# Kernel optimization log

Hardware: AMD Instinct MI355X
Metric: run time of the kernel (lower is better)

## Reference

```python
import jax, jax.numpy as jnp
import numpy as np

ALPHA = 1.702
LIMIT = 7.0
H = 2880      # hidden_size
D = 2880      # expert_dim (intermediate_size)
E = 8         # num_local_experts
B, S = 1, 1024


def setup_inputs() -> dict:
    key = jax.random.key(0)
    k1, k2, k3, k4, k5, k6 = jax.random.split(key, 6)
    scale = 1.0 / np.sqrt(H)
    return {
        "hidden_states": jax.random.normal(k1, (B, S, H), dtype=jnp.float32),
        "routing_weights": jax.random.uniform(k2, (B * S, E), dtype=jnp.float32),
        "gate_up_proj": jax.random.normal(k3, (E, H, 2 * D), dtype=jnp.float32) * scale,
        "gate_up_proj_bias": jax.random.normal(k4, (E, 2 * D), dtype=jnp.float32) * 0.02,
        "down_proj": jax.random.normal(k5, (E, D, H), dtype=jnp.float32) * (1.0 / np.sqrt(D)),
        "down_proj_bias": jax.random.normal(k6, (E, H), dtype=jnp.float32) * 0.02,
    }


def reference(hidden_states, routing_weights, gate_up_proj, gate_up_proj_bias,
              down_proj, down_proj_bias):
    b, s, h = hidden_states.shape
    x = hidden_states.reshape(-1, h)                       # [T, H]
    # Dense all-experts formulation (faithful to original): every expert sees every token.
    gate_up = jnp.einsum('th,ehd->etd', x, gate_up_proj) + gate_up_proj_bias[:, None, :]  # [E,T,2D]
    gate = gate_up[..., ::2]                               # interleaved split
    up = gate_up[..., 1::2]
    gate = jnp.minimum(gate, LIMIT)
    up = jnp.clip(up, -LIMIT, LIMIT)
    glu = gate * jax.nn.sigmoid(gate * ALPHA)
    out = jnp.einsum('etd,edh->eth', (up + 1.0) * glu, down_proj) + down_proj_bias[:, None, :]  # [E,T,H]
    # combine with routing weights: routing_weights [T,E] -> [E,T,1]
    out = out * routing_weights.T[:, :, None]
    y = out.sum(axis=0)                                    # [T, H]
    return y.reshape(b, s, h)
```

## Files before the change

### kernel.cpp

```cpp
#include <hip/hip_runtime.h>

namespace {

constexpr int T     = 1024;
constexpr int HDIM  = 2880;
constexpr int DDIM  = 2880;
constexpr int NE    = 8;
constexpr int TWO_D = 5760;
constexpr float ALPHA = 1.702f;
constexpr float LIMIT = 7.0f;

constexpr int LDSS = 40;

typedef __attribute__((ext_vector_type(8))) short bf16x8;
typedef __attribute__((ext_vector_type(4))) unsigned short u16x4;
typedef __attribute__((ext_vector_type(4))) float f32x4;

__device__ __forceinline__ unsigned short f2bf(float f) {
  union { float f; unsigned u; } x; x.f = f;
  unsigned u = x.u;
  u += 0x7fffu + ((u >> 16) & 1u);
  return (unsigned short)(u >> 16);
}

__device__ __forceinline__ void async16(const void* g, void* l) {
  __builtin_amdgcn_global_load_lds(
      (const __attribute__((address_space(1))) unsigned int*)g,
      (__attribute__((address_space(3))) unsigned int*)l, 16, 0, 0);
}

}


__global__ __launch_bounds__(256) void cvt_x_kernel(const float* __restrict__ X,
                                                    unsigned short* __restrict__ Xb) {
  const int i = (blockIdx.x * 256 + threadIdx.x) * 8;
  const f32x4 a = *(const f32x4*)(X + i);
  const f32x4 b = *(const f32x4*)(X + i + 4);
  bf16x8 pv;
  pv[0] = (short)f2bf(a.x); pv[1] = (short)f2bf(a.y);
  pv[2] = (short)f2bf(a.z); pv[3] = (short)f2bf(a.w);
  pv[4] = (short)f2bf(b.x); pv[5] = (short)f2bf(b.y);
  pv[6] = (short)f2bf(b.z); pv[7] = (short)f2bf(b.w);
  *(bf16x8*)(Xb + i) = pv;
}

__global__ __launch_bounds__(256) void transpose_cvt_kernel(
    const float* __restrict__ src, unsigned short* __restrict__ dst,
    int R, int C) {
  __shared__ __align__(16) unsigned short lt[64][70];
  const size_t eo = (size_t)blockIdx.z * R * C;
  const float* sp = src + eo;
  unsigned short* dp = dst + eo;
  const int c0 = blockIdx.x * 64;
  const int r0 = blockIdx.y * 64;
  const int t  = threadIdx.x;

  const int lr = t >> 4;
  const int lc = (t & 15) * 4;
#pragma unroll
  for (int it = 0; it < 4; ++it) {
    const int rr = lr + it * 16;
    const f32x4 v = *(const f32x4*)(sp + (size_t)(r0 + rr) * C + c0 + lc);
    const unsigned w0 = (unsigned)f2bf(v.x) | ((unsigned)f2bf(v.y) << 16);
    const unsigned w1 = (unsigned)f2bf(v.z) | ((unsigned)f2bf(v.w) << 16);
    *(unsigned*)(&lt[rr][lc])     = w0;
    *(unsigned*)(&lt[rr][lc + 2]) = w1;
  }
  __syncthreads();

  const int dr  = (t & 7) * 8;
  const int dcb = t >> 3;
#pragma unroll
  for (int it = 0; it < 2; ++it) {
    const int c = dcb + it * 32;
    bf16x8 ov;
#pragma unroll
    for (int j = 0; j < 8; ++j) ov[j] = (short)lt[dr + j][c];
    *(bf16x8*)(dp + (size_t)(c0 + c) * R + r0 + dr) = ov;
  }
}

__global__ __launch_bounds__(256) void gemm1_fast(
    const unsigned short* __restrict__ Xb,
    const unsigned short* __restrict__ W1T,
    const float* __restrict__ B1,
    const float* __restrict__ RW,
    unsigned short* __restrict__ A)
{
  __shared__ __align__(16) unsigned short lA[128 * 32];
  __shared__ __align__(16) unsigned short lB[128 * 32];

  const int tid = threadIdx.x;
  const int m0 = blockIdx.x * 128;
  const int n0 = blockIdx.y * 128;
  const int e  = blockIdx.z;
  const unsigned short* Wp = W1T + (size_t)e * TWO_D * HDIM;

  f32x4 acc[4][4];
#pragma unroll
  for (int i = 0; i < 4; ++i)
#pragma unroll
    for (int j = 0; j < 4; ++j) acc[i][j] = (f32x4)0.f;

  const int w    = tid >> 6;
  const int lane = tid & 63;
  const int wm   = w & 1, wn = w >> 1;
  const int r    = lane & 15, q = lane >> 4;

  const int srow = lane >> 2;
  const int skc  = (lane & 3) * 8;
  const unsigned short* ga = Xb + (size_t)(m0 + w * 32 + srow) * HDIM + skc;
  const unsigned short* gb = Wp + (size_t)(n0 + w * 32 + srow) * HDIM + skc;
  unsigned short* la0 = lA + (w * 2) * 512;
  unsigned short* lb0 = lB + (w * 2) * 512;

  for (int kt = 0; kt < HDIM / 32; ++kt) {
    const int k0 = kt * 32;
    async16(ga + k0,                        la0);
    async16(ga + (size_t)16 * HDIM + k0,    la0 + 512);
    async16(gb + k0,                        lb0);
    async16(gb + (size_t)16 * HDIM + k0,    lb0 + 512);
    __syncthreads();

    const unsigned short* pA = &lA[(wm * 64 + r) * 32 + q * 8];
    const unsigned short* pB = &lB[(wn * 64 + r) * 32 + q * 8];
    bf16x8 af[4], bfr[4];
#pragma unroll
    for (int i = 0; i < 4; ++i) af[i]  = *(const bf16x8*)(pA + i * 512);
#pragma unroll
    for (int j = 0; j < 4; ++j) bfr[j] = *(const bf16x8*)(pB + j * 512);
#pragma unroll
    for (int i = 0; i < 4; ++i)
#pragma unroll
      for (int j = 0; j < 4; ++j)
        acc[i][j] = __builtin_amdgcn_mfma_f32_16x16x32_bf16(af[i], bfr[j], acc[i][j], 0, 0, 0);

    __syncthreads();
  }

  const float* bp = B1 + (size_t)e * TWO_D;
#pragma unroll
  for (int i = 0; i < 4; ++i) {
    const int mb = m0 + wm * 64 + i * 16 + q * 4;
    float rwv[4];
#pragma unroll
    for (int p = 0; p < 4; ++p) rwv[p] = RW[(mb + p) * NE + e];
#pragma unroll
    for (int j = 0; j < 4; ++j) {
      const int c = n0 + wn * 64 + j * 16 + r;
      const float bias = bp[c];
#pragma unroll
      for (int p = 0; p < 4; ++p) {
        float v = acc[i][j][p] + bias;
        float o = __shfl_xor(v, 1, 64);
        float gate = (r & 1) ? o : v;
        float up   = (r & 1) ? v : o;
        gate = fminf(gate, LIMIT);
        up   = fminf(fmaxf(up, -LIMIT), LIMIT);
        float glu = gate / (1.f + __expf(-ALPHA * gate));
        float a   = (up + 1.f) * glu * rwv[p];
        if ((r & 1) == 0) {
          int d = c >> 1;
          A[(size_t)e * T * DDIM + (size_t)(mb + p) * DDIM + d] = f2bf(a);
        }
      }
    }
  }
}

__global__ __launch_bounds__(256) void gemm2_fast(
    const unsigned short* __restrict__ A,
    const unsigned short* __restrict__ W2T,
    float* __restrict__ Yp)
{
  __shared__ __align__(16) unsigned short lA[128 * 32];
  __shared__ __align__(16) unsigned short lB[128 * 32];

  const int tid = threadIdx.x;
  const int m0 = blockIdx.x * 128;
  const int n0 = blockIdx.y * 128;
  const int e  = blockIdx.z;
  const unsigned short* Ap = A   + (size_t)e * T * DDIM;
  const unsigned short* Wp = W2T + (size_t)e * HDIM * DDIM;

  f32x4 acc[4][4];
#pragma unroll
  for (int i = 0; i < 4; ++i)
#pragma unroll
    for (int j = 0; j < 4; ++j) acc[i][j] = (f32x4)0.f;

  const int w    = tid >> 6;
  const int lane = tid & 63;
  const int wm   = w & 1, wn = w >> 1;
  const int r    = lane & 15, q = lane >> 4;

  const int srow = lane >> 2;
  const int skc  = (lane & 3) * 8;
  int br0 = n0 + w * 32 + srow;
  int br1 = br0 + 16;
  if (br0 > HDIM - 1) br0 = HDIM - 1;
  if (br1 > HDIM - 1) br1 = HDIM - 1;
  const unsigned short* ga  = Ap + (size_t)(m0 + w * 32 + srow) * DDIM + skc;
  const unsigned short* gb0 = Wp + (size_t)br0 * DDIM + skc;
  const unsigned short* gb1 = Wp + (size_t)br1 * DDIM + skc;
  unsigned short* la0 = lA + (w * 2) * 512;
  unsigned short* lb0 = lB + (w * 2) * 512;

  for (int kt = 0; kt < DDIM / 32; ++kt) {
    const int k0 = kt * 32;
    async16(ga  + k0,                     la0);
    async16(ga  + (size_t)16 * DDIM + k0, la0 + 512);
    async16(gb0 + k0,                     lb0);
    async16(gb1 + k0,                     lb0 + 512);
    __syncthreads();

    const unsigned short* pA = &lA[(wm * 64 + r) * 32 + q * 8];
    const unsigned short* pB = &lB[(wn * 64 + r) * 32 + q * 8];
    bf16x8 af[4], bfr[4];
#pragma unroll
    for (int i = 0; i < 4; ++i) af[i]  = *(const bf16x8*)(pA + i * 512);
#pragma unroll
    for (int j = 0; j < 4; ++j) bfr[j] = *(const bf16x8*)(pB + j * 512);
#pragma unroll
    for (int i = 0; i < 4; ++i)
#pragma unroll
      for (int j = 0; j < 4; ++j)
        acc[i][j] = __builtin_amdgcn_mfma_f32_16x16x32_bf16(af[i], bfr[j], acc[i][j], 0, 0, 0);

    __syncthreads();
  }

#pragma unroll
  for (int i = 0; i < 4; ++i) {
    const int mb = m0 + wm * 64 + i * 16 + q * 4;
#pragma unroll
    for (int j = 0; j < 4; ++j) {
      const int h = n0 + wn * 64 + j * 16 + r;
      if (h < HDIM) {
#pragma unroll
        for (int p = 0; p < 4; ++p)
          Yp[((size_t)e * T + (mb + p)) * HDIM + h] = acc[i][j][p];
      }
    }
  }
}

__global__ __launch_bounds__(256) void reduce_bias_kernel(
    const float* __restrict__ Yp, const float* __restrict__ RW,
    const float* __restrict__ B2, float* __restrict__ Y) {
  const int idx = (blockIdx.x * 256 + threadIdx.x) * 4;
  const int t = idx / HDIM;
  const int h = idx - t * HDIM;
  f32x4 s = (f32x4)0.f;
#pragma unroll
  for (int e = 0; e < NE; ++e) {
    const f32x4 v = *(const f32x4*)(Yp + ((size_t)e * T + t) * HDIM + h);
    const f32x4 b = *(const f32x4*)(B2 + (size_t)e * HDIM + h);
    const float rw = RW[t * NE + e];
    s.x += v.x + rw * b.x;
    s.y += v.y + rw * b.y;
    s.z += v.z + rw * b.z;
    s.w += v.w + rw * b.w;
  }
  *(f32x4*)(Y + idx) = s;
}


__global__ void init_bias_kernel(const float* __restrict__ RW,
                                 const float* __restrict__ B2,
                                 float* __restrict__ Y) {
  int h = blockIdx.x * 64 + threadIdx.x;
  int t = blockIdx.y;
  float s = 0.f;
#pragma unroll
  for (int e = 0; e < NE; ++e) s += RW[t * NE + e] * B2[e * HDIM + h];
  Y[(size_t)t * HDIM + h] = s;
}

__global__ __launch_bounds__(256) void gemm1_act_kernel(
    const float* __restrict__ X, const float* __restrict__ W1,
    const float* __restrict__ B1, const float* __restrict__ RW,
    unsigned short* __restrict__ A) {
  __shared__ __align__(16) unsigned short lA[128 * LDSS];
  __shared__ __align__(16) unsigned short lB[128 * LDSS];
  const int tid = threadIdx.x;
  const int m0 = blockIdx.x * 128;
  const int n0 = blockIdx.y * 128;
  const int e  = blockIdx.z;
  const float* Wp = W1 + (size_t)e * HDIM * TWO_D;
  f32x4 acc[4][4];
#pragma unroll
  for (int i = 0; i < 4; ++i)
#pragma unroll
    for (int j = 0; j < 4; ++j) acc[i][j] = (f32x4)0.f;
  const int w = tid >> 6, lane = tid & 63;
  const int wm = w & 1, wn = w >> 1;
  const int r = lane & 15, q = lane >> 4;
  const int sa_m = tid >> 3, sa_q = tid & 7;
  const int sb_n = tid & 127, sb_k = tid >> 7;
  for (int kt = 0; kt < HDIM / 32; ++kt) {
    const int k0g = kt * 32;
#pragma unroll
    for (int it = 0; it < 4; ++it) {
      int m = sa_m + it * 32;
      const f32x4 v = *(const f32x4*)(X + (size_t)(m0 + m) * HDIM + k0g + sa_q * 4);
      u16x4 pv = { f2bf(v.x), f2bf(v.y), f2bf(v.z), f2bf(v.w) };
      *(u16x4*)(&lA[m * LDSS + sa_q * 4]) = pv;
    }
#pragma unroll
    for (int it = 0; it < 2; ++it) {
      int k0 = (sb_k + it * 2) * 8;
      float f[8];
#pragma unroll
      for (int rr = 0; rr < 8; ++rr)
        f[rr] = Wp[(size_t)(k0g + k0 + rr) * TWO_D + n0 + sb_n];
      bf16x8 pv = { (short)f2bf(f[0]), (short)f2bf(f[1]), (short)f2bf(f[2]), (short)f2bf(f[3]),
                    (short)f2bf(f[4]), (short)f2bf(f[5]), (short)f2bf(f[6]), (short)f2bf(f[7]) };
      *(bf16x8*)(&lB[sb_n * LDSS + k0]) = pv;
    }
    __syncthreads();
    const unsigned short* pA = &lA[(wm * 64 + r) * LDSS + q * 8];
    const unsigned short* pB = &lB[(wn * 64 + r) * LDSS + q * 8];
    bf16x8 af[4], bfr[4];
#pragma unroll
    for (int i = 0; i < 4; ++i) af[i]  = *(const bf16x8*)(pA + i * 16 * LDSS);
#pragma unroll
    for (int j = 0; j < 4; ++j) bfr[j] = *(const bf16x8*)(pB + j * 16 * LDSS);
#pragma unroll
    for (int i = 0; i < 4; ++i)
#pragma unroll
      for (int j = 0; j < 4; ++j)
        acc[i][j] = __builtin_amdgcn_mfma_f32_16x16x32_bf16(af[i], bfr[j], acc[i][j], 0, 0, 0);
    __syncthreads();
  }
  const float* bp = B1 + (size_t)e * TWO_D;
#pragma unroll
  for (int i = 0; i < 4; ++i) {
    const int mb = m0 + wm * 64 + i * 16 + q * 4;
    float rwv[4];
#pragma unroll
    for (int p = 0; p < 4; ++p) rwv[p] = RW[(mb + p) * NE + e];
#pragma unroll
    for (int j = 0; j < 4; ++j) {
      const int c = n0 + wn * 64 + j * 16 + r;
      const float bias = bp[c];
#pragma unroll
      for (int p = 0; p < 4; ++p) {
        float v = acc[i][j][p] + bias;
        float o = __shfl_xor(v, 1, 64);
        float gate = (r & 1) ? o : v;
        float up   = (r & 1) ? v : o;
        gate = fminf(gate, LIMIT);
        up   = fminf(fmaxf(up, -LIMIT), LIMIT);
        float glu = gate / (1.f + __expf(-ALPHA * gate));
        float a   = (up + 1.f) * glu * rwv[p];
        if ((r & 1) == 0) {
          int d = c >> 1;
          A[(size_t)e * T * DDIM + (size_t)(mb + p) * DDIM + d] = f2bf(a);
        }
      }
    }
  }
}

__global__ __launch_bounds__(256) void gemm2_acc_kernel(
    const unsigned short* __restrict__ A, const float* __restrict__ W2,
    float* __restrict__ Y) {
  __shared__ __align__(16) unsigned short lA[128 * LDSS];
  __shared__ __align__(16) unsigned short lB[128 * LDSS];
  const int tid = threadIdx.x;
  const int m0 = blockIdx.x * 128;
  const int n0 = blockIdx.y * 128;
  const int e  = blockIdx.z;
  const float* Wp = W2 + (size_t)e * DDIM * HDIM;
  const unsigned short* Ap = A + (size_t)e * T * DDIM;
  f32x4 acc[4][4];
#pragma unroll
  for (int i = 0; i < 4; ++i)
#pragma unroll
    for (int j = 0; j < 4; ++j) acc[i][j] = (f32x4)0.f;
  const int w = tid >> 6, lane = tid & 63;
  const int wm = w & 1, wn = w >> 1;
  const int r = lane & 15, q = lane >> 4;
  const int sa_m = tid >> 2, sa_c = tid & 3;
  const int sb_n = tid & 127, sb_k = tid >> 7;
  for (int kt = 0; kt < DDIM / 32; ++kt) {
    const int k0g = kt * 32;
#pragma unroll
    for (int it = 0; it < 2; ++it) {
      int m = sa_m + it * 64;
      bf16x8 v = *(const bf16x8*)(Ap + (size_t)(m0 + m) * DDIM + k0g + sa_c * 8);
      *(bf16x8*)(&lA[m * LDSS + sa_c * 8]) = v;
    }
    int col = n0 + sb_n;
    if (col > HDIM - 1) col = HDIM - 1;
#pragma unroll
    for (int it = 0; it < 2; ++it) {
      int k0 = (sb_k + it * 2) * 8;
      float f[8];
#pragma unroll
      for (int rr = 0; rr < 8; ++rr)
        f[rr] = Wp[(size_t)(k0g + k0 + rr) * HDIM + col];
      bf16x8 pv = { (short)f2bf(f[0]), (short)f2bf(f[1]), (short)f2bf(f[2]), (short)f2bf(f[3]),
                    (short)f2bf(f[4]), (short)f2bf(f[5]), (short)f2bf(f[6]), (short)f2bf(f[7]) };
      *(bf16x8*)(&lB[sb_n * LDSS + k0]) = pv;
    }
    __syncthreads();
    const unsigned short* pA = &lA[(wm * 64 + r) * LDSS + q * 8];
    const unsigned short* pB = &lB[(wn * 64 + r) * LDSS + q * 8];
    bf16x8 af[4], bfr[4];
#pragma unroll
    for (int i = 0; i < 4; ++i) af[i]  = *(const bf16x8*)(pA + i * 16 * LDSS);
#pragma unroll
    for (int j = 0; j < 4; ++j) bfr[j] = *(const bf16x8*)(pB + j * 16 * LDSS);
#pragma unroll
    for (int i = 0; i < 4; ++i)
#pragma unroll
      for (int j = 0; j < 4; ++j)
        acc[i][j] = __builtin_amdgcn_mfma_f32_16x16x32_bf16(af[i], bfr[j], acc[i][j], 0, 0, 0);
    __syncthreads();
  }
#pragma unroll
  for (int i = 0; i < 4; ++i) {
    const int mb = m0 + wm * 64 + i * 16 + q * 4;
#pragma unroll
    for (int j = 0; j < 4; ++j) {
      const int h = n0 + wn * 64 + j * 16 + r;
      if (h < HDIM) {
#pragma unroll
        for (int p = 0; p < 4; ++p)
          atomicAdd(&Y[(size_t)(mb + p) * HDIM + h], acc[i][j][p]);
      }
    }
  }
}

extern "C" void kernel_launch(void* const* d_in, const int* in_sizes, int n_in,
                              void* d_out, int out_size, void* d_ws, size_t ws_size,
                              hipStream_t stream) {
  const float* X  = (const float*)d_in[0];
  const float* RW = (const float*)d_in[1];
  const float* W1 = (const float*)d_in[2];
  const float* B1 = (const float*)d_in[3];
  const float* W2 = (const float*)d_in[4];
  const float* B2 = (const float*)d_in[5];
  float* Y = (float*)d_out;

  constexpr size_t XB_B  = (size_t)T * HDIM * 2;
  constexpr size_t AB_B  = (size_t)NE * T * DDIM * 2;
  constexpr size_t W1T_B = (size_t)NE * TWO_D * HDIM * 2;
  constexpr size_t W2T_B = (size_t)NE * HDIM * DDIM * 2;
  constexpr size_t YP_B  = (size_t)NE * T * HDIM * 4;
  constexpr size_t NEED  = XB_B + AB_B + W1T_B + W2T_B + YP_B;

  if (ws_size >= NEED) {
    char* p = (char*)d_ws;
    unsigned short* Xb  = (unsigned short*)p; p += XB_B;
    unsigned short* Ab  = (unsigned short*)p; p += AB_B;
    unsigned short* W1T = (unsigned short*)p; p += W1T_B;
    unsigned short* W2T = (unsigned short*)p; p += W2T_B;
    float* Yp = (float*)p;

    hipLaunchKernelGGL(cvt_x_kernel, dim3((T * HDIM) / 2048), dim3(256), 0, stream, X, Xb);
    hipLaunchKernelGGL(transpose_cvt_kernel, dim3(TWO_D / 64, HDIM / 64, NE), dim3(256), 0, stream,
                       W1, W1T, HDIM, TWO_D);
    hipLaunchKernelGGL(transpose_cvt_kernel, dim3(HDIM / 64, DDIM / 64, NE), dim3(256), 0, stream,
                       W2, W2T, DDIM, HDIM);
    hipLaunchKernelGGL(gemm1_fast, dim3(T / 128, TWO_D / 128, NE), dim3(256), 0, stream,
                       Xb, W1T, B1, RW, Ab);
    hipLaunchKernelGGL(gemm2_fast, dim3(T / 128, (HDIM + 127) / 128, NE), dim3(256), 0, stream,
                       Ab, W2T, Yp);
    hipLaunchKernelGGL(reduce_bias_kernel, dim3((T * HDIM) / 1024), dim3(256), 0, stream,
                       Yp, RW, B2, Y);
  } else {
    unsigned short* Abuf = (unsigned short*)d_ws;
    hipLaunchKernelGGL(init_bias_kernel, dim3(45, 1024), dim3(64), 0, stream, RW, B2, Y);
    hipLaunchKernelGGL(gemm1_act_kernel, dim3(8, 45, 8), dim3(256), 0, stream, X, W1, B1, RW, Abuf);
    hipLaunchKernelGGL(gemm2_acc_kernel, dim3(8, 23, 8), dim3(256), 0, stream, Abuf, W2, Y);
  }
}
```

Measured before the change: 1.556 ms.

## Rework weight transpose LDS layout and remap GEMM blocks for XCD locality

The transpose-convert kernel now packs pairs of rows into 32-bit words in a padded uint LDS tile, so that both the LDS reads and the global writes become 16-byte vectors instead of scalar 16-bit gathers. Both GEMM kernels remap the linear block id so that consecutive blocks scheduled on the same XCD (blocks are spread across eight) handle adjacent tiles of the same expert, aiming to improve L2 reuse of weight and activation tiles. The remap assumes fixed grid sizes (8x45x8 and 8x23x8) and would silently mis-map tiles if the launch grid differed.

Result: faster. 1.493 ms (-4.0%).

```diff
diff --git a/kernel.cpp b/kernel.cpp
--- a/kernel.cpp
+++ b/kernel.cpp
@@ -15,6 +15,7 @@
 typedef __attribute__((ext_vector_type(8))) short bf16x8;
 typedef __attribute__((ext_vector_type(4))) unsigned short u16x4;
 typedef __attribute__((ext_vector_type(4))) float f32x4;
+typedef __attribute__((ext_vector_type(4))) unsigned u32x4;
 
 __device__ __forceinline__ unsigned short f2bf(float f) {
   union { float f; unsigned u; } x; x.f = f;
@@ -48,7 +49,7 @@
 __global__ __launch_bounds__(256) void transpose_cvt_kernel(
     const float* __restrict__ src, unsigned short* __restrict__ dst,
     int R, int C) {
-  __shared__ __align__(16) unsigned short lt[64][70];
+  __shared__ unsigned lt32[64][33];
   const size_t eo = (size_t)blockIdx.z * R * C;
   const float* sp = src + eo;
   unsigned short* dp = dst + eo;
@@ -56,28 +57,38 @@
   const int r0 = blockIdx.y * 64;
   const int t  = threadIdx.x;
 
-  const int lr = t >> 4;
-  const int lc = (t & 15) * 4;
-#pragma unroll
-  for (int it = 0; it < 4; ++it) {
-    const int rr = lr + it * 16;
-    const f32x4 v = *(const f32x4*)(sp + (size_t)(r0 + rr) * C + c0 + lc);
-    const unsigned w0 = (unsigned)f2bf(v.x) | ((unsigned)f2bf(v.y) << 16);
-    const unsigned w1 = (unsigned)f2bf(v.z) | ((unsigned)f2bf(v.w) << 16);
-    *(unsigned*)(&lt[rr][lc])     = w0;
-    *(unsigned*)(&lt[rr][lc + 2]) = w1;
+  {
+    const int r2 = t >> 3;
+    const int cb = (t & 7) * 8;
+    const float* p0 = sp + (size_t)(r0 + 2 * r2) * C + c0 + cb;
+    const f32x4 a0 = *(const f32x4*)(p0);
+    const f32x4 a1 = *(const f32x4*)(p0 + 4);
+    const f32x4 b0 = *(const f32x4*)(p0 + C);
+    const f32x4 b1 = *(const f32x4*)(p0 + C + 4);
+    unsigned wv[8];
+    wv[0] = (unsigned)f2bf(a0.x) | ((unsigned)f2bf(b0.x) << 16);
+    wv[1] = (unsigned)f2bf(a0.y) | ((unsigned)f2bf(b0.y) << 16);
+    wv[2] = (unsigned)f2bf(a0.z) | ((unsigned)f2bf(b0.z) << 16);
+    wv[3] = (unsigned)f2bf(a0.w) | ((unsigned)f2bf(b0.w) << 16);
+    wv[4] = (unsigned)f2bf(a1.x) | ((unsigned)f2bf(b1.x) << 16);
+    wv[5] = (unsigned)f2bf(a1.y) | ((unsigned)f2bf(b1.y) << 16);
+    wv[6] = (unsigned)f2bf(a1.z) | ((unsigned)f2bf(b1.z) << 16);
+    wv[7] = (unsigned)f2bf(a1.w) | ((unsigned)f2bf(b1.w) << 16);
+#pragma unroll
+    for (int j = 0; j < 8; ++j) lt32[cb + j][r2] = wv[j];
   }
   __syncthreads();
-
-  const int dr  = (t & 7) * 8;
-  const int dcb = t >> 3;
-#pragma unroll
-  for (int it = 0; it < 2; ++it) {
-    const int c = dcb + it * 32;
-    bf16x8 ov;
-#pragma unroll
-    for (int j = 0; j < 8; ++j) ov[j] = (short)lt[dr + j][c];
-    *(bf16x8*)(dp + (size_t)(c0 + c) * R + r0 + dr) = ov;
+  {
+    const int c  = t >> 2;
+    const int rs = (t & 3) * 8;
+    unsigned o[8];
+#pragma unroll
+    for (int j = 0; j < 8; ++j) o[j] = lt32[c][rs + j];
+    unsigned short* q = dp + (size_t)(c0 + c) * R + r0 + 2 * rs;
+    u32x4 v0 = { o[0], o[1], o[2], o[3] };
+    u32x4 v1 = { o[4], o[5], o[6], o[7] };
+    *(u32x4*)(q)     = v0;
+    *(u32x4*)(q + 8) = v1;
   }
 }
 
@@ -92,9 +103,11 @@
   __shared__ __align__(16) unsigned short lB[128 * 32];
 
   const int tid = threadIdx.x;
-  const int m0 = blockIdx.x * 128;
-  const int n0 = blockIdx.y * 128;
-  const int e  = blockIdx.z;
+  const int bid = blockIdx.x + (blockIdx.y << 3) + blockIdx.z * 360;
+  const int lid = (bid & 7) * 360 + (bid >> 3);
+  const int m0 = (lid & 7) * 128;
+  const int n0 = ((lid >> 3) % 45) * 128;
+  const int e  = lid / 360;
   const unsigned short* Wp = W1T + (size_t)e * TWO_D * HDIM;
 
   f32x4 acc[4][4];
@@ -178,9 +191,11 @@
   __shared__ __align__(16) unsigned short lB[128 * 32];
 
   const int tid = threadIdx.x;
-  const int m0 = blockIdx.x * 128;
-  const int n0 = blockIdx.y * 128;
-  const int e  = blockIdx.z;
+  const int bid = blockIdx.x + (blockIdx.y << 3) + blockIdx.z * 184;
+  const int lid = (bid & 7) * 184 + (bid >> 3);
+  const int m0 = (lid & 7) * 128;
+  const int n0 = ((lid >> 3) % 23) * 128;
+  const int e  = lid / 184;
   const unsigned short* Ap = A   + (size_t)e * T * DDIM;
   const unsigned short* Wp = W2T + (size_t)e * HDIM * DDIM;
 
```
